# Performance work log

Measured on AMD Instinct MI355X. Metric: run time of the kernel, lower is better.

## Reference

```python
import jax, jax.numpy as jnp
import numpy as np

B, H, W = 1, 180, 360
NB, BS = 8, 96
EMBED = NB * BS            # 768
LATENT = 4 * EMBED         # 3072 (mlp_ratio=4)
MODD = 64
LAM = 0.01                 # sparsity_threshold (softshrink)

def _ln(x, w, b):
    m = x.mean(-1, keepdims=True)
    v = x.var(-1, keepdims=True)
    return (x - m) * jax.lax.rsqrt(v + 1e-5) * w + b

def _gelu(x):
    return jax.nn.gelu(x, approximate=False)  # torch nn.GELU default (erf)

def _scale_shift(e, w0, b0, w1, b1):
    o = _gelu(e @ w0 + b0) @ w1 + b1
    s, t = jnp.split(o, 2, axis=1)
    return 1.0 + s, t

def _softshrink(x):
    return jnp.where(x > LAM, x - LAM, jnp.where(x < -LAM, x + LAM, 0.0))

def _bd(x, w):  # block-diagonal contraction on spectral features
    return jnp.einsum('nyxbi,bio->nyxbo', x, w)

def _filter(x, e, w1, b1, w2, b2, fs_w0, fs_b0, fs_w1, fs_b1):
    bias = x
    b, h, w, c = x.shape
    xf = jnp.fft.rfft2(x, axes=(1, 2), norm='ortho')
    wf = w // 2 + 1
    xr = xf.real.reshape(b, h, wf, NB, BS)
    xi = xf.imag.reshape(b, h, wf, NB, BS)
    tm = min(h, w) // 2 + 1
    km = tm  # hard_thresholding_fraction = 1.0
    lo, hi = tm - km, min(tm + km, h)
    xrk, xik = xr[:, lo:hi, :km], xi[:, lo:hi, :km]
    o1r = _bd(xrk, w1[0]) - _bd(xik, w1[1]) + b1[0]
    o1i = _bd(xik, w1[0]) + _bd(xrk, w1[1]) + b1[1]
    s, t = _scale_shift(e, fs_w0, fs_b0, fs_w1, fs_b1)  # 'real' mode
    s = s.reshape(b, 1, 1, NB, BS)
    t = t.reshape(b, 1, 1, NB, BS)
    o1r = jax.nn.relu(o1r * s + t)
    o1i = jax.nn.relu(o1i * s + t)
    o2r = _softshrink(_bd(o1r, w2[0]) - _bd(o1i, w2[1]) + b2[0])
    o2i = _softshrink(_bd(o1i, w2[0]) + _bd(o1r, w2[1]) + b2[1])
    full = jnp.zeros((b, h, wf, NB, BS), jnp.complex64)
    full = full.at[:, lo:hi, :km].set(o2r + 1j * o2i)
    out = jnp.fft.irfft2(full.reshape(b, h, wf, c), s=(h, w), axes=(1, 2), norm='ortho')
    return out + bias

def _mlp(x, e, fc1w, fc1b, fc2w, fc2b, ms_w0, ms_b0, ms_w1, ms_b1):
    s, t = _scale_shift(e, ms_w0, ms_b0, ms_w1, ms_b1)
    s = s[:, None, None, :]
    t = t[:, None, None, :]
    hmid = _gelu((x @ fc1w + fc1b) * s + t)
    return hmid @ fc2w + fc2b

def setup_inputs():
    key = jax.random.key(0)
    ks = jax.random.split(key, 16)
    g = lambda k, shp: 0.02 * jax.random.normal(k, shp, jnp.float32)
    return {
        'x': jax.random.normal(ks[0], (B, H, W, EMBED), jnp.float32),
        'mod_embed': jax.random.normal(ks[1], (B, MODD), jnp.float32),
        'n1w': jnp.ones((EMBED,), jnp.float32),
        'n1b': jnp.zeros((EMBED,), jnp.float32),
        'n2w': jnp.ones((EMBED,), jnp.float32),
        'n2b': jnp.zeros((EMBED,), jnp.float32),
        'w1': g(ks[2], (2, NB, BS, BS)),
        'b1': g(ks[3], (2, NB, BS)),
        'w2': g(ks[4], (2, NB, BS, BS)),
        'b2': g(ks[5], (2, NB, BS)),
        'fs_w0': g(ks[6], (MODD, 2 * EMBED)),
        'fs_b0': jnp.zeros((2 * EMBED,), jnp.float32),
        'fs_w1': g(ks[7], (2 * EMBED, 2 * EMBED)),
        'fs_b1': jnp.zeros((2 * EMBED,), jnp.float32),
        'fc1w': g(ks[8], (EMBED, LATENT)),
        'fc1b': jnp.zeros((LATENT,), jnp.float32),
        'fc2w': g(ks[9], (LATENT, EMBED)),
        'fc2b': jnp.zeros((EMBED,), jnp.float32),
        'ms_w0': g(ks[10], (MODD, 2 * LATENT)),
        'ms_b0': jnp.zeros((2 * LATENT,), jnp.float32),
        'ms_w1': g(ks[11], (2 * LATENT, 2 * LATENT)),
        'ms_b1': jnp.zeros((2 * LATENT,), jnp.float32),
    }

def reference(x, mod_embed, n1w, n1b, n2w, n2b, w1, b1, w2, b2,
              fs_w0, fs_b0, fs_w1, fs_b1, fc1w, fc1b, fc2w, fc2b,
              ms_w0, ms_b0, ms_w1, ms_b1):
    residual = x
    h = _ln(x, n1w, n1b)
    h = _filter(h, mod_embed, w1, b1, w2, b2, fs_w0, fs_b0, fs_w1, fs_b1)
    h = h + residual            # double_skip = True
    residual = h
    h2 = _ln(h, n2w, n2b)
    h2 = _mlp(h2, mod_embed, fc1w, fc1b, fc2w, fc2b, ms_w0, ms_b0, ms_w1, ms_b1)
    return h2 + residual
```

## Files before the change

kernel.cpp:

```cpp
#include <hip/hip_runtime.h>
#include <hip/hip_bf16.h>
#include <math.h>

#define HH 180
#define WW 360
#define CC 768
#define FF 91
#define NPOS (HH*FF)
#define NROW (HH*WW)
#define LAT 3072

typedef __attribute__((ext_vector_type(8))) short bf16x8;
typedef __attribute__((ext_vector_type(4))) float f32x4;
typedef __attribute__((ext_vector_type(4))) unsigned int u32x4;

__device__ __forceinline__ float gelu_f(float x) {
    float u = 0.7978845608028654f * x * (1.0f + 0.044715f * x * x);
    float e = __expf(fminf(2.0f * u, 60.0f));
    return x * e / (e + 1.0f);
}

__global__ __launch_bounds__(256) void mod_a_kernel(
        const float* __restrict__ e,
        const float* __restrict__ fs_w0, const float* __restrict__ fs_b0,
        const float* __restrict__ ms_w0, const float* __restrict__ ms_b0,
        float* __restrict__ mid_f, float* __restrict__ mid_m) {
    __shared__ float es[64];
    int t = threadIdx.x;
    if (t < 64) es[t] = e[t];
    __syncthreads();
    int j = blockIdx.x * 256 + t;
    if (j < 1536) {
        float a = fs_b0[j];
        #pragma unroll 8
        for (int k = 0; k < 64; k++) a += es[k] * fs_w0[k*1536 + j];
        mid_f[j] = gelu_f(a);
    } else {
        int jm = j - 1536;
        float a = ms_b0[jm];
        #pragma unroll 8
        for (int k = 0; k < 64; k++) a += es[k] * ms_w0[k*6144 + jm];
        mid_m[jm] = gelu_f(a);
    }
}

__global__ __launch_bounds__(512) void mod_b_kernel(
        const float* __restrict__ mid_f, const float* __restrict__ mid_m,
        const float* __restrict__ fs_w1, const float* __restrict__ fs_b1,
        const float* __restrict__ ms_w1, const float* __restrict__ ms_b1,
        float* __restrict__ s_f, float* __restrict__ t_f,
        float* __restrict__ s_m, float* __restrict__ t_m) {
    __shared__ float red[8*64];
    int t = threadIdx.x;
    int g = t >> 6;
    int jl = t & 63;
    int blk = blockIdx.x;
    if (blk < 24) {
        int jo = blk*64 + jl;
        const int N = 1536, NQ = 192;
        float a = 0.f;
        const float* w = fs_w1 + (size_t)(g*NQ)*N + jo;
        for (int j = 0; j < NQ; j++) a += mid_f[g*NQ + j] * w[(size_t)j*N];
        red[t] = a;
        __syncthreads();
        if (t < 64) {
            float s = fs_b1[jo];
            #pragma unroll
            for (int q = 0; q < 8; q++) s += red[q*64 + jl];
            if (jo < 768) s_f[jo] = 1.0f + s;
            else          t_f[jo - 768] = s;
        }
    } else {
        int jo = (blk - 24)*64 + jl;
        const int N = 6144, NQ = 768;
        float a = 0.f;
        const float* w = ms_w1 + (size_t)(g*NQ)*N + jo;
        for (int j = 0; j < NQ; j++) a += mid_m[g*NQ + j] * w[(size_t)j*N];
        red[t] = a;
        __syncthreads();
        if (t < 64) {
            float s = ms_b1[jo];
            #pragma unroll
            for (int q = 0; q < 8; q++) s += red[q*64 + jl];
            if (jo < 3072) s_m[jo] = 1.0f + s;
            else           t_m[jo - 3072] = s;
        }
    }
}

__global__ __launch_bounds__(256) void ln_bf16_kernel(const float* __restrict__ in,
        const float* __restrict__ w, const float* __restrict__ b,
        __hip_bfloat16* __restrict__ out) {
    int row = blockIdx.x*4 + (threadIdx.x >> 6);
    int l = threadIdx.x & 63;
    const float* p = in + (size_t)row*CC;
    float v[12]; float s = 0.f, sq = 0.f;
    #pragma unroll
    for (int i = 0; i < 12; i++) { float tv = p[l + 64*i]; v[i] = tv; s += tv; sq += tv*tv; }
    #pragma unroll
    for (int m = 1; m < 64; m <<= 1) { s += __shfl_xor(s, m); sq += __shfl_xor(sq, m); }
    float mean = s * (1.0f/768.0f);
    float var  = sq * (1.0f/768.0f) - mean*mean;
    float rstd = rsqrtf(var + 1e-5f);
    __hip_bfloat16* o = out + (size_t)row*CC;
    #pragma unroll
    for (int i = 0; i < 12; i++) { int c = l + 64*i; o[c] = __float2bfloat16((v[i]-mean)*rstd*w[c] + b[c]); }
}

__global__ __launch_bounds__(256) void ew_kernel(__hip_bfloat16* __restrict__ Ew) {
    int idx = blockIdx.x*256 + threadIdx.x;
    if (idx >= 192*384) return;
    int r = idx / 384, w = idx - (idx/384)*384;
    int f = (r < 96) ? r : r - 96;
    const float rn = 0.05270462766947299f;
    float v = 0.f;
    if (f < FF && w < WW) {
        int p = (f * w) % 360;
        float ang = 6.283185307179586f/360.0f * (float)p;
        float s_, c_; sincosf(ang, &s_, &c_);
        v = (r < 96) ? c_*rn : -s_*rn;
    }
    Ew[idx] = __float2bfloat16(v);
}

__global__ __launch_bounds__(256) void eh_kernel(__hip_bfloat16* __restrict__ Eh) {
    int idx = blockIdx.x*256 + threadIdx.x;
    if (idx >= 4*192*384) return;
    int sp = idx / (192*384);
    int rem = idx - sp*(192*384);
    int t = rem / 384, k = rem - (rem/384)*384;
    int sig = sp >> 1, plane = sp & 1;
    float s = (sig == 0) ? -1.f : 1.f;
    int h = (k < 192) ? k : k - 192;
    const float rnh = 0.07453559924999299f;
    float v = 0.f;
    if (t < HH && h < HH) {
        int p = (t * h) % 180;
        float ang = 6.283185307179586f/180.0f * (float)p;
        float s_, c_; sincosf(ang, &s_, &c_);
        float C = c_*rnh, S = s_*rnh;
        if (plane == 0) v = (k < 192) ? C : -s*S;
        else            v = (k < 192) ? s*S : C;
    }
    Eh[idx] = __float2bfloat16(v);
}

__global__ __launch_bounds__(256) void bdw_kernel(const float* __restrict__ w,
        __hip_bfloat16* __restrict__ Bt) {
    int idx = blockIdx.x*256 + threadIdx.x;
    if (idx >= 8*192*192) return;
    int wb = idx / (192*192);
    int rem = idx - wb*(192*192);
    int n2 = rem / 192, k2 = rem - (rem/192)*192;
    int k = (k2 < 96) ? k2 : k2 - 96;
    int oc = (n2 < 96) ? n2 : n2 - 96;
    float w0 = w[((size_t)wb*96 + k)*96 + oc];
    float w1v = w[((size_t)(8 + wb)*96 + k)*96 + oc];
    float v;
    if (n2 < 96) v = (k2 < 96) ? w0 : -w1v;
    else         v = (k2 < 96) ? w1v : w0;
    Bt[idx] = __float2bfloat16(v);
}

template<int MODE, int BSRC>
__global__ __launch_bounds__(256) void transform_mfma(
        const __hip_bfloat16* __restrict__ Amat,
        const float* __restrict__ B0, const float* __restrict__ B1,
        float* __restrict__ O0, float* __restrict__ O1) {
    __shared__ __align__(16) unsigned short As[192*72];
    __shared__ __align__(16) unsigned short Bs[128*72];
    int nbase = blockIdx.x * 128;
    int bat = blockIdx.z;
    int tid = threadIdx.x;
    int l = tid & 63, wv = tid >> 6;
    int wm = wv & 1, wn = wv >> 1;
    int lm = l & 15, kq = l >> 4;
    const __hip_bfloat16* Ab = Amat + (MODE == 1 ? (size_t)blockIdx.y*192*384 : 0);
    size_t bRowStride = (MODE == 0) ? (size_t)CC : (size_t)FF*CC;
    size_t bBase      = (MODE == 0) ? (size_t)bat*WW*CC : (size_t)bat*CC;
    f32x4 acc[6][4] = {};
    for (int kt = 0; kt < 6; kt++) {
        int kb = kt*64;
        __syncthreads();
        #pragma unroll
        for (int it = 0; it < 6; it++) {
            int ch = it*256 + tid;
            int row = ch >> 3, co = (ch & 7) * 8;
            u32x4 v = *(const u32x4*)(Ab + (size_t)row*384 + kb + co);
            *(u32x4*)(As + row*72 + co) = v;
        }
        if (MODE == 0 && BSRC == 1) {
            const __hip_bfloat16* Bb = (const __hip_bfloat16*)B0;
            #pragma unroll
            for (int it = 0; it < 4; it++) {
                int idx = it*256 + tid;
                int row = idx >> 4;
                int cq = (idx & 15) * 8;
                int k = kb + row;
                unsigned int u[4] = {0u, 0u, 0u, 0u};
                if (k < WW) {
                    u32x4 v = *(const u32x4*)(Bb + bBase + (size_t)k*bRowStride + nbase + cq);
                    u[0] = v[0]; u[1] = v[1]; u[2] = v[2]; u[3] = v[3];
                }
                #pragma unroll
                for (int j = 0; j < 4; j++) {
                    Bs[(cq + 2*j    )*72 + row] = (unsigned short)(u[j] & 0xffffu);
                    Bs[(cq + 2*j + 1)*72 + row] = (unsigned short)(u[j] >> 16);
                }
            }
        } else {
            #pragma unroll
            for (int it = 0; it < 8; it++) {
                int idx = it*256 + tid;
                int row = idx >> 5;
                int cq = (idx & 31) * 4;
                int k = kb + row;
                float4 v = make_float4(0.f, 0.f, 0.f, 0.f);
                if (MODE == 0) {
                    if (k < WW) v = *(const float4*)(B0 + bBase + (size_t)k*bRowStride + nbase + cq);
                } else {
                    if (k < 192) { if (k < HH) v = *(const float4*)(B0 + bBase + (size_t)k*bRowStride + nbase + cq); }
                    else { int h2 = k - 192; if (h2 < HH) v = *(const float4*)(B1 + bBase + (size_t)h2*bRowStride + nbase + cq); }
                }
                __hip_bfloat16 b0 = __float2bfloat16(v.x);
                __hip_bfloat16 b1 = __float2bfloat16(v.y);
                __hip_bfloat16 b2 = __float2bfloat16(v.z);
                __hip_bfloat16 b3 = __float2bfloat16(v.w);
                Bs[(cq+0)*72 + row] = *reinterpret_cast<unsigned short*>(&b0);
                Bs[(cq+1)*72 + row] = *reinterpret_cast<unsigned short*>(&b1);
                Bs[(cq+2)*72 + row] = *reinterpret_cast<unsigned short*>(&b2);
                Bs[(cq+3)*72 + row] = *reinterpret_cast<unsigned short*>(&b3);
            }
        }
        __syncthreads();
        #pragma unroll
        for (int kk = 0; kk < 2; kk++) {
            int kg = kk*32 + kq*8;
            bf16x8 af[6], bfv[4];
            #pragma unroll
            for (int i = 0; i < 6; i++)
                af[i] = *(const bf16x8*)(As + (wm*96 + i*16 + lm)*72 + kg);
            #pragma unroll
            for (int j = 0; j < 4; j++)
                bfv[j] = *(const bf16x8*)(Bs + (wn*64 + j*16 + lm)*72 + kg);
            #pragma unroll
            for (int i = 0; i < 6; i++)
                #pragma unroll
                for (int j = 0; j < 4; j++)
                    acc[i][j] = __builtin_amdgcn_mfma_f32_16x16x32_bf16(af[i], bfv[j], acc[i][j], 0, 0, 0);
        }
    }
    int r0 = kq * 4;
    #pragma unroll
    for (int j = 0; j < 4; j++) {
        int col = nbase + wn*64 + j*16 + lm;
        #pragma unroll
        for (int i = 0; i < 6; i++) {
            #pragma unroll
            for (int r = 0; r < 4; r++) {
                int row = wm*96 + i*16 + r0 + r;
                float v = acc[i][j][r];
                if (MODE == 0) {
                    if (row < 96) {
                        if (row < FF) O0[(size_t)bat*FF*CC + (size_t)row*CC + col] = v;
                    } else {
                        int f2 = row - 96;
                        if (f2 < FF) O1[(size_t)bat*FF*CC + (size_t)f2*CC + col] = v;
                    }
                } else {
                    if (row < HH) {
                        float* Op = blockIdx.y ? O1 : O0;
                        Op[(size_t)row*FF*CC + (size_t)bat*CC + col] = v;
                    }
                }
            }
        }
    }
}

template<int LAYER>
__global__ __launch_bounds__(384) void bd_mfma_kernel(
        const float* __restrict__ Ir, const float* __restrict__ Ii,
        const __hip_bfloat16* __restrict__ Bt,
        const float* __restrict__ bias,
        const float* __restrict__ sf, const float* __restrict__ tf,
        float* __restrict__ Or_, float* __restrict__ Oi_) {
    __shared__ __align__(16) unsigned short As[128*72];
    __shared__ __align__(16) unsigned short Bs[192*72];
    int mbase = blockIdx.x * 128;
    int wb = blockIdx.y;
    int tid = threadIdx.x;
    int l = tid & 63, wv = tid >> 6;
    int wm = wv & 1, wn = wv >> 1;
    int lm = l & 15, kq = l >> 4;
    const __hip_bfloat16* Bw = Bt + (size_t)wb*192*192;
    f32x4 acc[4][4] = {};
    for (int kt = 0; kt < 3; kt++) {
        __syncthreads();
        for (int ch = tid; ch < 2048; ch += 384) {
            int row = ch >> 4, q = ch & 15;
            int k2 = kt*64 + q*4;
            int p = mbase + row; if (p >= NPOS) p = NPOS - 1;
            const float* src = (k2 < 96) ? (Ir + (size_t)p*CC + wb*96 + k2)
                                         : (Ii + (size_t)p*CC + wb*96 + (k2 - 96));
            float4 v = *(const float4*)src;
            __hip_bfloat16 b0 = __float2bfloat16(v.x);
            __hip_bfloat16 b1 = __float2bfloat16(v.y);
            __hip_bfloat16 b2 = __float2bfloat16(v.z);
            __hip_bfloat16 b3 = __float2bfloat16(v.w);
            unsigned int lo = (unsigned int)*reinterpret_cast<unsigned short*>(&b0)
                            | ((unsigned int)*reinterpret_cast<unsigned short*>(&b1) << 16);
            unsigned int hi = (unsigned int)*reinterpret_cast<unsigned short*>(&b2)
                            | ((unsigned int)*reinterpret_cast<unsigned short*>(&b3) << 16);
            *(uint2*)(As + row*72 + q*4) = make_uint2(lo, hi);
        }
        for (int ch = tid; ch < 1536; ch += 384) {
            int row = ch >> 3, co = (ch & 7) * 8;
            u32x4 v = *(const u32x4*)(Bw + (size_t)row*192 + kt*64 + co);
            *(u32x4*)(Bs + row*72 + co) = v;
        }
        __syncthreads();
        #pragma unroll
        for (int kk = 0; kk < 2; kk++) {
            int kg = kk*32 + kq*8;
            bf16x8 af[4], bfv[4];
            #pragma unroll
            for (int i = 0; i < 4; i++) {
                af[i]  = *(const bf16x8*)(As + (wm*64 + i*16 + lm)*72 + kg);
                bfv[i] = *(const bf16x8*)(Bs + (wn*64 + i*16 + lm)*72 + kg);
            }
            #pragma unroll
            for (int i = 0; i < 4; i++)
                #pragma unroll
                for (int j = 0; j < 4; j++)
                    acc[i][j] = __builtin_amdgcn_mfma_f32_16x16x32_bf16(af[i], bfv[j], acc[i][j], 0, 0, 0);
        }
    }
    int r0 = kq * 4;
    #pragma unroll
    for (int j = 0; j < 4; j++) {
        int n2 = wn*64 + j*16 + lm;
        int oc = (n2 < 96) ? n2 : n2 - 96;
        float bb = bias[((n2 < 96) ? 0 : 768) + wb*96 + oc];
        float ss = 0.f, tt = 0.f;
        if (LAYER == 0) { ss = sf[wb*96 + oc]; tt = tf[wb*96 + oc]; }
        float* Op = (n2 < 96) ? Or_ : Oi_;
        #pragma unroll
        for (int i = 0; i < 4; i++) {
            #pragma unroll
            for (int r = 0; r < 4; r++) {
                int p = mbase + wm*64 + i*16 + r0 + r;
                if (p < NPOS) {
                    float v = acc[i][j][r] + bb;
                    if (LAYER == 0) {
                        v = fmaxf(v*ss + tt, 0.0f);
                    } else {
                        v = (v > 0.01f) ? (v - 0.01f) : ((v < -0.01f) ? (v + 0.01f) : 0.0f);
                    }
                    Op[(size_t)p*CC + wb*96 + oc] = v;
                }
            }
        }
    }
}

__global__ __launch_bounds__(256) void aw_kernel(__hip_bfloat16* __restrict__ Aw) {
    int idx = blockIdx.x*256 + threadIdx.x;
    if (idx >= 384*96) return;
    int w = idx / 96, f = idx - (idx/96)*96;
    const float rn = 0.05270462766947299f;
    float m = (f == 0) ? rn : ((f < FF) ? 2.0f*rn : 0.0f);
    int p = (int)(((long long)f * w) % 360);
    float ang = 6.283185307179586f / 360.0f * (float)p;
    float s_, c_; sincosf(ang, &s_, &c_);
    Aw[idx]          = __float2bfloat16(m * c_);
    Aw[384*96 + idx] = __float2bfloat16(-m * s_);
}

__global__ __launch_bounds__(256) void iwdft_mfma_kernel(
        const float* __restrict__ Zr, const float* __restrict__ Zi,
        const __hip_bfloat16* __restrict__ Aw,
        const __hip_bfloat16* __restrict__ hlnb,
        const float* __restrict__ xin, float* __restrict__ hout) {
    __shared__ __align__(16) unsigned short As[128*104];
    __shared__ __align__(16) unsigned short Bs[128*104];
    int h = blockIdx.z;
    int mbase = blockIdx.y * 128;
    int nbase = blockIdx.x * 128;
    int tid = threadIdx.x;
    int l = tid & 63, wv = tid >> 6;
    int wm = wv & 1, wn = wv >> 1;
    int lm = l & 15, kq = l >> 4;
    f32x4 acc[4][4] = {};
    #pragma unroll
    for (int ph = 0; ph < 2; ph++) {
        __syncthreads();
        for (int ch = tid; ch < 1536; ch += 256) {
            int row = ch / 12, co = (ch - row*12) * 8;
            u32x4 v = *(const u32x4*)(Aw + ((size_t)ph*384 + mbase + row)*96 + co);
            *(u32x4*)(As + row*104 + co) = v;
        }
        const float* Zp = ph ? Zi : Zr;
        for (int ch = tid; ch < 96*32; ch += 256) {
            int f = ch >> 5, cg = (ch & 31) * 4;
            float4 v;
            if (f < FF) v = *(const float4*)(Zp + ((size_t)h*FF + f)*CC + nbase + cg);
            else        v = make_float4(0.f, 0.f, 0.f, 0.f);
            __hip_bfloat16 b0 = __float2bfloat16(v.x);
            __hip_bfloat16 b1 = __float2bfloat16(v.y);
            __hip_bfloat16 b2 = __float2bfloat16(v.z);
            __hip_bfloat16 b3 = __float2bfloat16(v.w);
            Bs[(cg+0)*104 + f] = *reinterpret_cast<unsigned short*>(&b0);
            Bs[(cg+1)*104 + f] = *reinterpret_cast<unsigned short*>(&b1);
            Bs[(cg+2)*104 + f] = *reinterpret_cast<unsigned short*>(&b2);
            Bs[(cg+3)*104 + f] = *reinterpret_cast<unsigned short*>(&b3);
        }
        __syncthreads();
        #pragma unroll
        for (int ks = 0; ks < 3; ks++) {
            int kg = ks*32 + kq*8;
            bf16x8 af[4], bfv[4];
            #pragma unroll
            for (int i = 0; i < 4; i++) {
                af[i]  = *(const bf16x8*)(As + (wm*64 + i*16 + lm)*104 + kg);
                bfv[i] = *(const bf16x8*)(Bs + (wn*64 + i*16 + lm)*104 + kg);
            }
            #pragma unroll
            for (int i = 0; i < 4; i++)
                #pragma unroll
                for (int j = 0; j < 4; j++)
                    acc[i][j] = __builtin_amdgcn_mfma_f32_16x16x32_bf16(af[i], bfv[j], acc[i][j], 0, 0, 0);
        }
    }
    int r0 = kq * 4;
    #pragma unroll
    for (int j = 0; j < 4; j++) {
        int col = nbase + wn*64 + j*16 + lm;
        #pragma unroll
        for (int i = 0; i < 4; i++) {
            int rowb = wm*64 + i*16 + r0;
            #pragma unroll
            for (int r = 0; r < 4; r++) {
                int wp = mbase + rowb + r;
                if (wp < WW) {
                    size_t idx = ((size_t)h*WW + wp)*CC + col;
                    hout[idx] = acc[i][j][r] + __bfloat162float(hlnb[idx]) + xin[idx];
                }
            }
        }
    }
}

__global__ __launch_bounds__(256) void transpose_bf16_kernel(const float* __restrict__ src,
        __hip_bfloat16* __restrict__ dst, int K, int N) {
    __shared__ float tile[32][33];
    int n0 = blockIdx.x * 32;
    int k0 = blockIdx.y * 32;
    int tx = threadIdx.x & 31;
    int ty = threadIdx.x >> 5;
    #pragma unroll
    for (int r = 0; r < 32; r += 8) {
        tile[ty + r][tx] = src[(size_t)(k0 + ty + r) * N + n0 + tx];
    }
    __syncthreads();
    #pragma unroll
    for (int r = 0; r < 32; r += 8) {
        dst[(size_t)(n0 + ty + r) * K + k0 + tx] = __float2bfloat16(tile[tx][ty + r]);
    }
}

template<int MODE>
__global__ __launch_bounds__(256) void gemm_kernel(
        const __hip_bfloat16* __restrict__ A,
        const __hip_bfloat16* __restrict__ Bt,
        int M, int K, int N,
        const float* __restrict__ bias,
        const float* __restrict__ sv, const float* __restrict__ tv,
        const float* resid, void* out) {
    __shared__ __align__(16) unsigned short SH[128*136];
    unsigned short* As = SH;
    unsigned short* Bs = SH + 128*64;
    int tid = threadIdx.x;
    int nbase = blockIdx.x * 128;
    int mbase = blockIdx.y * 128;
    int l = tid & 63, wv = tid >> 6;
    int wm = wv & 1, wn = wv >> 1;
    int lm = l & 15;
    int kq = l >> 4;
    f32x4 acc[4][4] = {};
    int nkt = K >> 6;
    for (int kt = 0; kt < nkt; kt++) {
        int kb = kt << 6;
        __syncthreads();
        #pragma unroll
        for (int i = 0; i < 4; i++) {
            int ch = i*256 + tid;
            int row = ch >> 3;
            int sl = ch & 7;
            int kg = (sl ^ (row & 7)) << 3;
            int am = mbase + row; if (am >= M) am = M - 1;
            const __hip_bfloat16* ga = A  + (size_t)am * K + kb + kg;
            const __hip_bfloat16* gb = Bt + (size_t)(nbase + row) * K + kb + kg;
            __builtin_amdgcn_global_load_lds(
                (const __attribute__((address_space(1))) void*)(unsigned long long)(uintptr_t)ga,
                (__attribute__((address_space(3))) void*)(unsigned long long)(uintptr_t)(As + ch*8),
                16, 0, 0);
            __builtin_amdgcn_global_load_lds(
                (const __attribute__((address_space(1))) void*)(unsigned long long)(uintptr_t)gb,
                (__attribute__((address_space(3))) void*)(unsigned long long)(uintptr_t)(Bs + ch*8),
                16, 0, 0);
        }
        __syncthreads();
        #pragma unroll
        for (int kk = 0; kk < 2; kk++) {
            bf16x8 af[4], bfv[4];
            #pragma unroll
            for (int i = 0; i < 4; i++) {
                int ra = wm*64 + i*16 + lm;
                af[i]  = *(const bf16x8*)(As + ra*64 + ((((kk<<2)+kq) ^ (ra&7))<<3));
                int rb = wn*64 + i*16 + lm;
                bfv[i] = *(const bf16x8*)(Bs + rb*64 + ((((kk<<2)+kq) ^ (rb&7))<<3));
            }
            #pragma unroll
            for (int i = 0; i < 4; i++)
                #pragma unroll
                for (int j = 0; j < 4; j++)
                    acc[i][j] = __builtin_amdgcn_mfma_f32_16x16x32_bf16(af[i], bfv[j], acc[i][j], 0, 0, 0);
        }
    }
    int r0 = kq * 4;
    if (MODE == 0) {
        __syncthreads();
        #pragma unroll
        for (int j = 0; j < 4; j++) {
            int col = wn*64 + j*16 + lm;
            int gcol = nbase + col;
            float bb = bias[gcol];
            float ss = sv[gcol], tt = tv[gcol];
            #pragma unroll
            for (int i = 0; i < 4; i++) {
                int rowb = wm*64 + i*16 + r0;
                #pragma unroll
                for (int r = 0; r < 4; r++) {
                    float v = gelu_f((acc[i][j][r] + bb)*ss + tt);
                    __hip_bfloat16 hb = __float2bfloat16(v);
                    SH[(rowb + r)*136 + col] = *reinterpret_cast<unsigned short*>(&hb);
                }
            }
        }
        __syncthreads();
        #pragma unroll
        for (int it = 0; it < 8; it++) {
            int chunk = it*256 + tid;
            int row = chunk >> 4;
            int c8 = chunk & 15;
            int mr = mbase + row;
            if (mr < M) {
                *(u32x4*)((__hip_bfloat16*)out + (size_t)mr*N + nbase + c8*8) =
                    *(const u32x4*)(SH + row*136 + c8*8);
            }
        }
    } else {
        #pragma unroll
        for (int j = 0; j < 4; j++) {
            int col = nbase + wn*64 + j*16 + lm;
            float bb = bias[col];
            #pragma unroll
            for (int i = 0; i < 4; i++) {
                int rowb = mbase + wm*64 + i*16 + r0;
                #pragma unroll
                for (int r = 0; r < 4; r++) {
                    int row = rowb + r;
                    if (row < M) {
                        float v = acc[i][j][r] + bb;
                        ((float*)out)[(size_t)row*N + col] = v + resid[(size_t)row*N + col];
                    }
                }
            }
        }
    }
}

extern "C" void kernel_launch(void* const* d_in, const int* in_sizes, int n_in,
                              void* d_out, int out_size, void* d_ws, size_t ws_size,
                              hipStream_t stream) {
    const float* x     = (const float*)d_in[0];
    const float* emb   = (const float*)d_in[1];
    const float* n1w   = (const float*)d_in[2];
    const float* n1b   = (const float*)d_in[3];
    const float* n2w   = (const float*)d_in[4];
    const float* n2b   = (const float*)d_in[5];
    const float* w1    = (const float*)d_in[6];
    const float* b1    = (const float*)d_in[7];
    const float* w2    = (const float*)d_in[8];
    const float* b2    = (const float*)d_in[9];
    const float* fs_w0 = (const float*)d_in[10];
    const float* fs_b0 = (const float*)d_in[11];
    const float* fs_w1 = (const float*)d_in[12];
    const float* fs_b1 = (const float*)d_in[13];
    const float* fc1w  = (const float*)d_in[14];
    const float* fc1b  = (const float*)d_in[15];
    const float* fc2w  = (const float*)d_in[16];
    const float* fc2b  = (const float*)d_in[17];
    const float* ms_w0 = (const float*)d_in[18];
    const float* ms_b0 = (const float*)d_in[19];
    const float* ms_w1 = (const float*)d_in[20];
    const float* ms_b1 = (const float*)d_in[21];
    float* out = (float*)d_out;
    (void)in_sizes; (void)n_in; (void)out_size; (void)ws_size;

    char* wsb = (char*)d_ws;
    size_t off = 0;
    auto alloc = [&](size_t nbytes) -> void* {
        void* p = wsb + off;
        off += (nbytes + 255) & ~(size_t)255;
        return p;
    };
    float* s_f  = (float*)alloc(768*4);
    float* t_f  = (float*)alloc(768*4);
    float* s_m  = (float*)alloc(3072*4);
    float* t_m  = (float*)alloc(3072*4);
    float* midf = (float*)alloc(1536*4);
    float* midm = (float*)alloc(6144*4);
    __hip_bfloat16* Aw  = (__hip_bfloat16*)alloc((size_t)2*384*96*2);
    __hip_bfloat16* Ew  = (__hip_bfloat16*)alloc((size_t)192*384*2);
    __hip_bfloat16* Eh  = (__hip_bfloat16*)alloc((size_t)4*192*384*2);
    __hip_bfloat16* Bt1 = (__hip_bfloat16*)alloc((size_t)8*192*192*2);
    __hip_bfloat16* Bt2 = (__hip_bfloat16*)alloc((size_t)8*192*192*2);
    float* Yr   = (float*)alloc((size_t)NPOS*CC*4);
    float* Yi   = (float*)alloc((size_t)NPOS*CC*4);
    float* Zr   = (float*)alloc((size_t)NPOS*CC*4);
    float* Zi   = (float*)alloc((size_t)NPOS*CC*4);
    __hip_bfloat16* wT1  = (__hip_bfloat16*)alloc((size_t)CC*LAT*2);
    __hip_bfloat16* wT2  = (__hip_bfloat16*)alloc((size_t)CC*LAT*2);
    __hip_bfloat16* h2   = (__hip_bfloat16*)alloc((size_t)NROW*CC*2);
    __hip_bfloat16* hmid = (__hip_bfloat16*)alloc((size_t)NROW*LAT*2);
    __hip_bfloat16* hlnb = h2;

    mod_a_kernel<<<30, 256, 0, stream>>>(emb, fs_w0, fs_b0, ms_w0, ms_b0, midf, midm);
    mod_b_kernel<<<120, 512, 0, stream>>>(midf, midm, fs_w1, fs_b1, ms_w1, ms_b1,
                                          s_f, t_f, s_m, t_m);
    aw_kernel<<<144, 256, 0, stream>>>(Aw);
    ew_kernel<<<288, 256, 0, stream>>>(Ew);
    eh_kernel<<<1152, 256, 0, stream>>>(Eh);
    bdw_kernel<<<1152, 256, 0, stream>>>(w1, Bt1);
    bdw_kernel<<<1152, 256, 0, stream>>>(w2, Bt2);
    ln_bf16_kernel<<<NROW/4, 256, 0, stream>>>(x, n1w, n1b, hlnb);
    transpose_bf16_kernel<<<dim3(LAT/32, CC/32), 256, 0, stream>>>(fc1w, wT1, 768, 3072);
    transpose_bf16_kernel<<<dim3(CC/32, LAT/32), 256, 0, stream>>>(fc2w, wT2, 3072, 768);

    transform_mfma<0,1><<<dim3(6, 1, 180), 256, 0, stream>>>(Ew, (const float*)hlnb, nullptr, Yr, Yi);
    transform_mfma<1,0><<<dim3(6, 2, 91), 256, 0, stream>>>(Eh, Yr, Yi, Zr, Zi);
    bd_mfma_kernel<0><<<dim3(128, 8), 384, 0, stream>>>(Zr, Zi, Bt1, b1, s_f, t_f, Yr, Yi);
    bd_mfma_kernel<1><<<dim3(128, 8), 384, 0, stream>>>(Yr, Yi, Bt2, b2, nullptr, nullptr, Zr, Zi);
    transform_mfma<1,0><<<dim3(6, 2, 91), 256, 0, stream>>>(Eh + (size_t)2*192*384, Zr, Zi, Yr, Yi);
    iwdft_mfma_kernel<<<dim3(6, 3, 180), 256, 0, stream>>>(Yr, Yi, Aw, hlnb, x, out);

    ln_bf16_kernel<<<NROW/4, 256, 0, stream>>>(out, n2w, n2b, h2);
    gemm_kernel<0><<<dim3(LAT/128, (NROW+127)/128), 256, 0, stream>>>(
        h2, wT1, NROW, CC, LAT, fc1b, s_m, t_m, nullptr, hmid);
    gemm_kernel<1><<<dim3(CC/128, (NROW+127)/128), 256, 0, stream>>>(
        hmid, wT2, NROW, LAT, CC, fc2b, nullptr, nullptr, out, out);
}
```

Baseline: 2.162 ms.

## Use 256x256 double-buffered GEMM tiles with 512 threads and erf GELU

Replaces the 128x128 MLP GEMM with a 256x256 tile kernel of 512 threads (8 waves, each computing 128x64). It double-buffers the LDS stages so the next K-tile loads while MFMAs run, and drops one barrier per iteration. Larger tiles raise operand reuse and cut global traffic, but use 128KB of LDS per block, which limits occupancy and may make launch_bounds(512,2) unachievable. GELU also switches from the tanh approximation to exact erf, matching the reference at a higher ALU cost in the epilogue.

```diff
diff --git a/kernel.cpp b/kernel.cpp
--- a/kernel.cpp
+++ b/kernel.cpp
@@ -15,9 +15,7 @@
 typedef __attribute__((ext_vector_type(4))) unsigned int u32x4;
 
 __device__ __forceinline__ float gelu_f(float x) {
-    float u = 0.7978845608028654f * x * (1.0f + 0.044715f * x * x);
-    float e = __expf(fminf(2.0f * u, 60.0f));
-    return x * e / (e + 1.0f);
+    return 0.5f * x * (1.0f + erff(x * 0.7071067811865476f));
 }
 
 __global__ __launch_bounds__(256) void mod_a_kernel(
@@ -470,31 +468,30 @@
 }
 
 template<int MODE>
-__global__ __launch_bounds__(256) void gemm_kernel(
+__global__ __launch_bounds__(512, 2) void gemm256_kernel(
         const __hip_bfloat16* __restrict__ A,
         const __hip_bfloat16* __restrict__ Bt,
         int M, int K, int N,
         const float* __restrict__ bias,
         const float* __restrict__ sv, const float* __restrict__ tv,
         const float* resid, void* out) {
-    __shared__ __align__(16) unsigned short SH[128*136];
-    unsigned short* As = SH;
-    unsigned short* Bs = SH + 128*64;
+    __shared__ __align__(16) unsigned short SH[65536];
+    unsigned short* Asb = SH;
+    unsigned short* Bsb = SH + 32768;
     int tid = threadIdx.x;
-    int nbase = blockIdx.x * 128;
-    int mbase = blockIdx.y * 128;
+    int nbase = blockIdx.x * 256;
+    int mbase = blockIdx.y * 256;
     int l = tid & 63, wv = tid >> 6;
     int wm = wv & 1, wn = wv >> 1;
-    int lm = l & 15;
-    int kq = l >> 4;
-    f32x4 acc[4][4] = {};
+    int lm = l & 15, kq = l >> 4;
+    f32x4 acc[8][4] = {};
     int nkt = K >> 6;
-    for (int kt = 0; kt < nkt; kt++) {
+
+    auto stage = [&](int d, int kt) {
         int kb = kt << 6;
-        __syncthreads();
         #pragma unroll
         for (int i = 0; i < 4; i++) {
-            int ch = i*256 + tid;
+            int ch = i*512 + tid;
             int row = ch >> 3;
             int sl = ch & 7;
             int kg = (sl ^ (row & 7)) << 3;
@@ -503,34 +500,46 @@
             const __hip_bfloat16* gb = Bt + (size_t)(nbase + row) * K + kb + kg;
             __builtin_amdgcn_global_load_lds(
                 (const __attribute__((address_space(1))) void*)(unsigned long long)(uintptr_t)ga,
-                (__attribute__((address_space(3))) void*)(unsigned long long)(uintptr_t)(As + ch*8),
+                (__attribute__((address_space(3))) void*)(unsigned long long)(uintptr_t)(Asb + d*16384 + ch*8),
                 16, 0, 0);
             __builtin_amdgcn_global_load_lds(
                 (const __attribute__((address_space(1))) void*)(unsigned long long)(uintptr_t)gb,
-                (__attribute__((address_space(3))) void*)(unsigned long long)(uintptr_t)(Bs + ch*8),
+                (__attribute__((address_space(3))) void*)(unsigned long long)(uintptr_t)(Bsb + d*16384 + ch*8),
                 16, 0, 0);
         }
-        __syncthreads();
+    };
+
+    stage(0, 0);
+    __syncthreads();
+    for (int kt = 0; kt < nkt; kt++) {
+        if (kt + 1 < nkt) stage((kt + 1) & 1, kt + 1);
+        int d = kt & 1;
+        const unsigned short* Ab = Asb + d*16384;
+        const unsigned short* Bb = Bsb + d*16384;
         #pragma unroll
         for (int kk = 0; kk < 2; kk++) {
-            bf16x8 af[4], bfv[4];
-            #pragma unroll
-            for (int i = 0; i < 4; i++) {
-                int ra = wm*64 + i*16 + lm;
-                af[i]  = *(const bf16x8*)(As + ra*64 + ((((kk<<2)+kq) ^ (ra&7))<<3));
-                int rb = wn*64 + i*16 + lm;
-                bfv[i] = *(const bf16x8*)(Bs + rb*64 + ((((kk<<2)+kq) ^ (rb&7))<<3));
-            }
-            #pragma unroll
-            for (int i = 0; i < 4; i++)
+            bf16x8 af[8], bfv[4];
+            #pragma unroll
+            for (int i = 0; i < 8; i++) {
+                int ra = wm*128 + i*16 + lm;
+                af[i] = *(const bf16x8*)(Ab + ra*64 + ((((kk<<2)+kq) ^ (ra&7))<<3));
+            }
+            #pragma unroll
+            for (int j = 0; j < 4; j++) {
+                int rb = wn*64 + j*16 + lm;
+                bfv[j] = *(const bf16x8*)(Bb + rb*64 + ((((kk<<2)+kq) ^ (rb&7))<<3));
+            }
+            #pragma unroll
+            for (int i = 0; i < 8; i++)
                 #pragma unroll
                 for (int j = 0; j < 4; j++)
                     acc[i][j] = __builtin_amdgcn_mfma_f32_16x16x32_bf16(af[i], bfv[j], acc[i][j], 0, 0, 0);
         }
-    }
+        __syncthreads();
+    }
+
     int r0 = kq * 4;
     if (MODE == 0) {
-        __syncthreads();
         #pragma unroll
         for (int j = 0; j < 4; j++) {
             int col = wn*64 + j*16 + lm;
@@ -538,26 +547,26 @@
             float bb = bias[gcol];
             float ss = sv[gcol], tt = tv[gcol];
             #pragma unroll
-            for (int i = 0; i < 4; i++) {
-                int rowb = wm*64 + i*16 + r0;
+            for (int i = 0; i < 8; i++) {
+                int rowb = wm*128 + i*16 + r0;
                 #pragma unroll
                 for (int r = 0; r < 4; r++) {
                     float v = gelu_f((acc[i][j][r] + bb)*ss + tt);
                     __hip_bfloat16 hb = __float2bfloat16(v);
-                    SH[(rowb + r)*136 + col] = *reinterpret_cast<unsigned short*>(&hb);
-                }
-            }
-        }
-        __syncthreads();
-        #pragma unroll
-        for (int it = 0; it < 8; it++) {
-            int chunk = it*256 + tid;
-            int row = chunk >> 4;
-            int c8 = chunk & 15;
+                    SH[(rowb + r)*256 + col] = *reinterpret_cast<unsigned short*>(&hb);
+                }
+            }
+        }
+        __syncthreads();
+        #pragma unroll
+        for (int it = 0; it < 16; it++) {
+            int chunk = it*512 + tid;
+            int row = chunk >> 5;
+            int c8 = chunk & 31;
             int mr = mbase + row;
             if (mr < M) {
                 *(u32x4*)((__hip_bfloat16*)out + (size_t)mr*N + nbase + c8*8) =
-                    *(const u32x4*)(SH + row*136 + c8*8);
+                    *(const u32x4*)(SH + row*256 + c8*8);
             }
         }
     } else {
@@ -566,8 +575,8 @@
             int col = nbase + wn*64 + j*16 + lm;
             float bb = bias[col];
             #pragma unroll
-            for (int i = 0; i < 4; i++) {
-                int rowb = mbase + wm*64 + i*16 + r0;
+            for (int i = 0; i < 8; i++) {
+                int rowb = mbase + wm*128 + i*16 + r0;
                 #pragma unroll
                 for (int r = 0; r < 4; r++) {
                     int row = rowb + r;
@@ -657,8 +666,8 @@
     iwdft_mfma_kernel<<<dim3(6, 3, 180), 256, 0, stream>>>(Yr, Yi, Aw, hlnb, x, out);
 
     ln_bf16_kernel<<<NROW/4, 256, 0, stream>>>(out, n2w, n2b, h2);
-    gemm_kernel<0><<<dim3(LAT/128, (NROW+127)/128), 256, 0, stream>>>(
+    gemm256_kernel<0><<<dim3(LAT/256, (NROW+255)/256), 512, 0, stream>>>(
         h2, wT1, NROW, CC, LAT, fc1b, s_m, t_m, nullptr, hmid);
-    gemm_kernel<1><<<dim3(CC/128, (NROW+127)/128), 256, 0, stream>>>(
+    gemm256_kernel<1><<<dim3(CC/256, (NROW+255)/256), 512, 0, stream>>>(
         hmid, wT2, NROW, LAT, CC, fc2b, nullptr, nullptr, out, out);
 }
```

New measurement: 2.031 ms. 6.1% less time.
